# Kernel tuning notes

Hardware: AMD Instinct MI355X
Metric: run time of the kernel (lower is better)

## Reference

```python
import jax, jax.numpy as jnp
import numpy as np

# Conv2dfft forward (no spectral compression: preserve_energy=None, index_back=None, out_size=None)
# Implements cross-correlation (DL convolution) via rfft2 / irfft2, matching the torch module's
# padding and output-size logic:
#   out_H = H - HH + 1 + 2*pad ; init_fft = H + 2*pad + max(out_H, HH) - 1

PAD = 1  # padding from init_kwargs


def setup_inputs() -> dict:
    key = jax.random.key(0)
    k1, k2, k3 = jax.random.split(key, 3)
    x = jax.random.normal(k1, (32, 128, 32, 32), dtype=jnp.float32)
    w = jax.random.normal(k2, (128, 128, 3, 3), dtype=jnp.float32) * 0.1
    b = jax.random.normal(k3, (128,), dtype=jnp.float32)
    return {"x": x, "w": w, "b": b}


def reference(x, w, b):
    N, C, H, W = x.shape
    F, _, HH, WW = w.shape
    out_H = H - HH + 1 + 2 * PAD
    out_W = W - WW + 1 + 2 * PAD
    init_fft_H = H + 2 * PAD + max(out_H, HH) - 1  # 65
    init_fft_W = W + 2 * PAD + max(out_W, WW) - 1  # 65

    # pad input: explicit conv padding + zero-pad up to FFT grid
    fft_pad_H = init_fft_H - 2 * PAD - H
    fft_pad_W = init_fft_W - 2 * PAD - W
    px = jnp.pad(x, ((0, 0), (0, 0), (PAD, PAD + fft_pad_H), (PAD, PAD + fft_pad_W)))
    pw = jnp.pad(w, ((0, 0), (0, 0), (0, init_fft_H - HH), (0, init_fft_W - WW)))

    xfft = jnp.fft.rfft2(px)                     # [N,C,65,33] complex64
    yfft = jnp.fft.rfft2(pw)                     # [F,C,65,33] complex64

    # cross-correlation: multiply by conj(filter fft), accumulate over input channels
    prod = jnp.einsum('nchw,fchw->nfhw', xfft, jnp.conj(yfft))
    full = jnp.fft.irfft2(prod, s=(init_fft_H, init_fft_W))  # [N,F,65,65]
    out = full[:, :, :out_H, :out_W] + b[None, :, None, None]
    return out
```

## Files before the change

kernel.cpp:

```cpp
#include <hip/hip_runtime.h>


typedef __attribute__((ext_vector_type(8))) short bf16x8;
typedef __attribute__((ext_vector_type(4))) float f32x4;

#define N_IMG 32
#define C_IN  128
#define F_OUT 128
#define HW    32
#define HPAD  34

__device__ __forceinline__ unsigned short f2bf(float f) {
    union { float f; unsigned u; } v; v.f = f;
    unsigned r = v.u + 0x7fffu + ((v.u >> 16) & 1u);
    return (unsigned short)(r >> 16);
}

__global__ __launch_bounds__(256) void pack_x_kernel(const float* __restrict__ x,
                                                     unsigned short* __restrict__ xp) {
    __shared__ unsigned short tile[C_IN * HPAD];
    const int n   = blockIdx.x / HPAD;
    const int hp  = blockIdx.x - n * HPAD;
    const int tid = threadIdx.x;
    const unsigned base_out = (unsigned)(n * HPAD + hp) * (HPAD * C_IN);
    if (hp >= 1 && hp <= 32) {
        const int h = hp - 1;
        #pragma unroll
        for (int i = 0; i < 16; ++i) {
            int idx = tid + i * 256;
            int c = idx >> 5, w = idx & 31;
            tile[c * HPAD + (w + 1)] = f2bf(x[((n * C_IN + c) * HW + h) * HW + w]);
        }
        if (tid < C_IN) { tile[tid * HPAD] = 0; tile[tid * HPAD + 33] = 0; }
        __syncthreads();
        #pragma unroll
        for (int i = 0; i < 17; ++i) {
            int idx = tid + i * 256;
            int wp = idx >> 7, c = idx & 127;
            xp[base_out + (unsigned)idx] = tile[c * HPAD + wp];
        }
    } else {
        #pragma unroll
        for (int i = 0; i < 17; ++i) {
            int idx = tid + i * 256;
            xp[base_out + (unsigned)idx] = 0;
        }
    }
}

__global__ __launch_bounds__(256) void pack_w_kernel(const float* __restrict__ w,
                                                     unsigned short* __restrict__ wpk) {
    int idx = blockIdx.x * 256 + threadIdx.x;
    int ci = idx & 31;
    int f  = (idx >> 5) & 127;
    int u  = idx >> 12;
    int cc = u / 9;
    int t  = u - cc * 9;
    wpk[idx] = f2bf(w[(f * C_IN + cc * 32 + ci) * 9 + t]);
}

__global__ __launch_bounds__(256, 2) void conv_gemm_kernel(
    const unsigned short* __restrict__ xp,
    const unsigned short* __restrict__ wpk,
    const float* __restrict__ bias,
    float* __restrict__ out)
{
    __shared__ alignas(16) unsigned short lds_x[1024 * 8];
    __shared__ alignas(16) unsigned short lds_a[2304 * 8];

    const int tid  = threadIdx.x;
    const int lane = tid & 63;
    const int wave = tid >> 6;
    const int qk   = lane >> 4;
    const int l15  = lane & 15;

    const int fh   = blockIdx.x & 1;
    const int band = (blockIdx.x >> 1) & 7;
    const int n    = blockIdx.x >> 4;
    const int f0   = fh * 64;
    const int h0   = band * 4;

    f32x4 acc[4][2];
    #pragma unroll
    for (int mi = 0; mi < 4; ++mi)
        #pragma unroll
        for (int ni = 0; ni < 2; ++ni)
            acc[mi][ni] = (f32x4){0.f, 0.f, 0.f, 0.f};

    const int a_lane = l15 * 32 + (((qk ^ (l15 >> 1)) & 3) << 3);
    int brow0[2];
    #pragma unroll
    for (int ni = 0; ni < 2; ++ni)
        brow0[ni] = wave * HPAD + ni * 16 + l15;

    const unsigned short* xsrc0 = xp + (unsigned)((n * HPAD + h0) * HPAD) * C_IN;
    const unsigned short* wbase = wpk + f0 * 32;

    for (int cc = 0; cc < 4; ++cc) {
        __syncthreads();
        #pragma unroll
        for (int i = 0; i < 4; ++i) {
            int p = tid + i * 256;
            int row = p >> 2;  if (row > 203) row = 203;
            int lc = (p ^ (row >> 1)) & 3;
            const unsigned short* src = xsrc0 + row * C_IN + cc * 32 + lc * 8;
            __builtin_amdgcn_global_load_lds(
                (const __attribute__((address_space(1))) void*)src,
                (__attribute__((address_space(3))) void*)(&lds_x[p * 8]),
                16, 0, 0);
        }
        const unsigned short* wsrc = wbase + cc * 36864;
        #pragma unroll
        for (int j = 0; j < 9; ++j) {
            int q = tid + j * 256;
            int row = q >> 2;
            int lc = (q ^ (row >> 1)) & 3;
            const unsigned short* src = wsrc + ((row >> 6) * 4096) + ((row & 63) * 32) + lc * 8;
            __builtin_amdgcn_global_load_lds(
                (const __attribute__((address_space(1))) void*)src,
                (__attribute__((address_space(3))) void*)(&lds_a[q * 8]),
                16, 0, 0);
        }
        __syncthreads();
        #pragma unroll
        for (int tap = 0; tap < 9; ++tap) {
            const int r = tap / 3, s = tap - 3 * (tap / 3);
            bf16x8 af[4], bf[2];
            #pragma unroll
            for (int mi = 0; mi < 4; ++mi)
                af[mi] = *(const bf16x8*)&lds_a[tap * 2048 + mi * 512 + a_lane];
            #pragma unroll
            for (int ni = 0; ni < 2; ++ni) {
                int row = brow0[ni] + (r * HPAD + s);
                int el  = (row << 5) + (((qk ^ (row >> 1)) & 3) << 3);
                bf[ni] = *(const bf16x8*)&lds_x[el];
            }
            #pragma unroll
            for (int mi = 0; mi < 4; ++mi)
                #pragma unroll
                for (int ni = 0; ni < 2; ++ni)
                    acc[mi][ni] = __builtin_amdgcn_mfma_f32_16x16x32_bf16(
                        af[mi], bf[ni], acc[mi][ni], 0, 0, 0);
        }
    }

    const int h = h0 + wave;
    #pragma unroll
    for (int mi = 0; mi < 4; ++mi) {
        const int f_base = f0 + mi * 16 + qk * 4;
        float bv[4];
        #pragma unroll
        for (int r2 = 0; r2 < 4; ++r2) bv[r2] = bias[f_base + r2];
        #pragma unroll
        for (int ni = 0; ni < 2; ++ni) {
            const int w2 = ni * 16 + l15;
            #pragma unroll
            for (int r2 = 0; r2 < 4; ++r2) {
                out[((unsigned)(n * F_OUT + f_base + r2) * HW + h) * HW + w2] =
                    acc[mi][ni][r2] + bv[r2];
            }
        }
    }
}

extern "C" void kernel_launch(void* const* d_in, const int* in_sizes, int n_in,
                              void* d_out, int out_size, void* d_ws, size_t ws_size,
                              hipStream_t stream) {
    const float* x = (const float*)d_in[0];
    const float* w = (const float*)d_in[1];
    const float* b = (const float*)d_in[2];
    float* out = (float*)d_out;

    unsigned short* xp  = (unsigned short*)d_ws;
    unsigned short* wpk = xp + (size_t)N_IMG * HPAD * HPAD * C_IN;

    pack_x_kernel<<<N_IMG * HPAD, 256, 0, stream>>>(x, xp);
    pack_w_kernel<<<576, 256, 0, stream>>>(w, wpk);
    conv_gemm_kernel<<<512, 256, 0, stream>>>(xp, wpk, b, out);
}
```

Measured before the change: 88.73 us.

## Stage full input band in LDS once and read weights directly from global

The conv GEMM now loads the whole 6-row input halo band for all 128 channels into LDS once, using a 16-chunk XOR swizzle, instead of reloading a 32-channel slice for each of the four channel chunks. Weight fragments are read straight from global memory (through the cache) into registers rather than staged in LDS. This drops the per-chunk barriers and removes the weight LDS buffer. In exchange, weight loads hit global/L2 latency inside the MFMA loop with no overlap. The larger input LDS buffer (about 53KB) may also limit occupancy.

```diff
diff --git a/kernel.cpp b/kernel.cpp
--- a/kernel.cpp
+++ b/kernel.cpp
@@ -65,8 +65,7 @@
     const float* __restrict__ bias,
     float* __restrict__ out)
 {
-    __shared__ alignas(16) unsigned short lds_x[1024 * 8];
-    __shared__ alignas(16) unsigned short lds_a[2304 * 8];
+    __shared__ alignas(16) unsigned short lds_x[208 * C_IN];
 
     const int tid  = threadIdx.x;
     const int lane = tid & 63;
@@ -80,6 +79,19 @@
     const int f0   = fh * 64;
     const int h0   = band * 4;
 
+    const unsigned short* xbase = xp + (unsigned)((n * HPAD + h0) * HPAD) * C_IN;
+    #pragma unroll
+    for (int i = 0; i < 13; ++i) {
+        int p = tid + i * 256;
+        int row = p >> 4;  if (row > 203) row = 203;
+        int lc = (p ^ row) & 15;
+        const unsigned short* src = xbase + row * C_IN + lc * 8;
+        __builtin_amdgcn_global_load_lds(
+            (const __attribute__((address_space(1))) void*)src,
+            (__attribute__((address_space(3))) void*)(&lds_x[p * 8]),
+            16, 0, 0);
+    }
+
     f32x4 acc[4][2];
     #pragma unroll
     for (int mi = 0; mi < 4; ++mi)
@@ -87,53 +99,29 @@
         for (int ni = 0; ni < 2; ++ni)
             acc[mi][ni] = (f32x4){0.f, 0.f, 0.f, 0.f};
 
-    const int a_lane = l15 * 32 + (((qk ^ (l15 >> 1)) & 3) << 3);
-    int brow0[2];
+    const unsigned short* wbase = wpk + f0 * 32 + l15 * 32 + qk * 8;
+
+    const int rrb0 = wave * HPAD + l15;
+    const int rrb1 = wave * HPAD + 16 + l15;
+
+    __syncthreads();
+
     #pragma unroll
-    for (int ni = 0; ni < 2; ++ni)
-        brow0[ni] = wave * HPAD + ni * 16 + l15;
-
-    const unsigned short* xsrc0 = xp + (unsigned)((n * HPAD + h0) * HPAD) * C_IN;
-    const unsigned short* wbase = wpk + f0 * 32;
-
     for (int cc = 0; cc < 4; ++cc) {
-        __syncthreads();
-        #pragma unroll
-        for (int i = 0; i < 4; ++i) {
-            int p = tid + i * 256;
-            int row = p >> 2;  if (row > 203) row = 203;
-            int lc = (p ^ (row >> 1)) & 3;
-            const unsigned short* src = xsrc0 + row * C_IN + cc * 32 + lc * 8;
-            __builtin_amdgcn_global_load_lds(
-                (const __attribute__((address_space(1))) void*)src,
-                (__attribute__((address_space(3))) void*)(&lds_x[p * 8]),
-                16, 0, 0);
-        }
-        const unsigned short* wsrc = wbase + cc * 36864;
-        #pragma unroll
-        for (int j = 0; j < 9; ++j) {
-            int q = tid + j * 256;
-            int row = q >> 2;
-            int lc = (q ^ (row >> 1)) & 3;
-            const unsigned short* src = wsrc + ((row >> 6) * 4096) + ((row & 63) * 32) + lc * 8;
-            __builtin_amdgcn_global_load_lds(
-                (const __attribute__((address_space(1))) void*)src,
-                (__attribute__((address_space(3))) void*)(&lds_a[q * 8]),
-                16, 0, 0);
-        }
-        __syncthreads();
         #pragma unroll
         for (int tap = 0; tap < 9; ++tap) {
             const int r = tap / 3, s = tap - 3 * (tap / 3);
             bf16x8 af[4], bf[2];
             #pragma unroll
             for (int mi = 0; mi < 4; ++mi)
-                af[mi] = *(const bf16x8*)&lds_a[tap * 2048 + mi * 512 + a_lane];
-            #pragma unroll
-            for (int ni = 0; ni < 2; ++ni) {
-                int row = brow0[ni] + (r * HPAD + s);
-                int el  = (row << 5) + (((qk ^ (row >> 1)) & 3) << 3);
-                bf[ni] = *(const bf16x8*)&lds_x[el];
+                af[mi] = *(const bf16x8*)(wbase + cc * 36864 + tap * 4096 + mi * 512);
+            {
+                int rr0 = rrb0 + r * HPAD + s;
+                int ph0 = (cc * 4 + qk) ^ (rr0 & 15);
+                bf[0] = *(const bf16x8*)&lds_x[rr0 * C_IN + ph0 * 8];
+                int rr1 = rrb1 + r * HPAD + s;
+                int ph1 = (cc * 4 + qk) ^ (rr1 & 15);
+                bf[1] = *(const bf16x8*)&lds_x[rr1 * C_IN + ph1 * 8];
             }
             #pragma unroll
             for (int mi = 0; mi < 4; ++mi)
```

Measured after the change: 101.0 us. 1.14x slower.
